# Kernel tuning notes

Hardware: AMD Instinct MI355X
Metric: run time of the kernel (lower is better)

Reference implementation:

```python
import jax, jax.numpy as jnp
import numpy as np

T, P, E, H = 256, 256, 300, 256   # seq, batch(paragraphs), embed, lstm_size
M, C = 50000, 16384               # pair occurrences / candidates per type
MT, CT = 50000, 16384             # triple occurrences / candidates


def setup_inputs() -> dict:
    key = jax.random.key(0)
    ks = jax.random.split(key, 32)
    f = lambda i, shape, s=0.05: jax.random.normal(ks[i], shape, dtype=jnp.float32) * s
    inp = {
        "x": jax.random.normal(ks[0], (T, P, E), dtype=jnp.float32),
        # BiLSTM params (pytorch gate order i,f,g,o; b = b_ih + b_hh)
        "wih_f": f(1, (4 * H, E)), "whh_f": f(2, (4 * H, H)), "b_f": f(3, (4 * H,)),
        "wih_b": f(4, (4 * H, E)), "whh_b": f(5, (4 * H, H)), "b_b": f(6, (4 * H,)),
        # per-pair-type (drug-gene, drug-variant, gene-variant) stacked params
        "pair_hW": f(7, (3, 4 * H, 2 * H)), "pair_hb": f(8, (3, 2 * H)),
        "pair_oW": f(9, (3, 2 * H)), "pair_ob": f(10, (3,)),
        "pair_backoff": f(11, (3, 2 * H)),
        "tri_hW": f(12, (6 * H, 2 * H)), "tri_hb": f(13, (2 * H,)),
        "tri_backoff": f(14, (2 * H,)),
        "all_hW": f(15, (8 * H, 2 * H)), "all_hb": f(16, (2 * H,)),
        "out_tW": f(17, (2 * H,)), "out_tb": f(18, ()),
        # flattened (t*P+p) indices of mention starts, per pair type
        "occ1": jax.random.randint(ks[19], (3, M), 0, T * P, dtype=jnp.int32),
        "occ2": jax.random.randint(ks[20], (3, M), 0, T * P, dtype=jnp.int32),
        "seg": jax.random.randint(ks[21], (3, M), 0, C, dtype=jnp.int32),
        "tri_occ1": jax.random.randint(ks[22], (MT,), 0, T * P, dtype=jnp.int32),
        "tri_occ2": jax.random.randint(ks[23], (MT,), 0, T * P, dtype=jnp.int32),
        "tri_occ3": jax.random.randint(ks[24], (MT,), 0, T * P, dtype=jnp.int32),
        "tri_seg": jax.random.randint(ks[25], (MT,), 0, CT, dtype=jnp.int32),
        # pair candidate index looked up for each triple after removing entity i
        "tri_pair_idx": jax.random.randint(ks[26], (CT, 3), 0, C, dtype=jnp.int32),
    }
    return inp


def _lstm_dir(x, wih, whh, b):
    """Unidirectional LSTM over leading time axis. x: [T, P, E] -> [T, P, H]."""
    Pb, Hh = x.shape[1], whh.shape[1]
    def step(carry, xt):
        h, c = carry
        g = xt @ wih.T + h @ whh.T + b               # [P, 4H]
        i, fgate, gg, o = jnp.split(g, 4, axis=-1)
        c = jax.nn.sigmoid(fgate) * c + jax.nn.sigmoid(i) * jnp.tanh(gg)
        h = jax.nn.sigmoid(o) * jnp.tanh(c)
        return (h, c), h
    init = (jnp.zeros((Pb, Hh), x.dtype), jnp.zeros((Pb, Hh), x.dtype))
    _, hs = jax.lax.scan(step, init, x)
    return hs


def _forward(x, wih_f, whh_f, b_f, wih_b, whh_b, b_b, pair_hW, pair_hb, pair_oW,
             pair_ob, pair_backoff, tri_hW, tri_hb, tri_backoff, all_hW, all_hb,
             out_tW, out_tb, occ1, occ2, seg, tri_occ1, tri_occ2, tri_occ3,
             tri_seg, tri_pair_idx):
    hf = _lstm_dir(x, wih_f, whh_f, b_f)
    hb = _lstm_dir(x[::-1], wih_b, whh_b, b_b)[::-1]
    embs = jnp.concatenate([hf, hb], axis=-1)        # [T, P, 2H]
    flat = embs.reshape(-1, embs.shape[-1])          # [T*P, 2H]

    pair_vecs, pair_logits = [], []
    for k in range(3):  # fixed set of entity-type pairs
        v = jnp.concatenate([flat[occ1[k]], flat[occ2[k]]], axis=-1)   # [M, 4H]
        reps = v @ pair_hW[k] + pair_hb[k]                             # [M, 2H]
        counts = jax.ops.segment_sum(jnp.ones((reps.shape[0],), reps.dtype),
                                     seg[k], num_segments=C)
        pooled = jax.ops.segment_max(reps, seg[k], num_segments=C)
        pooled = jnp.where(counts[:, None] > 0, pooled, pair_backoff[k])
        pv = jnp.tanh(pooled)                                          # [C, 2H]
        pair_vecs.append(pv)
        pair_logits.append(pv @ pair_oW[k] + pair_ob[k])               # [C]

    tv = jnp.concatenate([flat[tri_occ1], flat[tri_occ2], flat[tri_occ3]], axis=-1)
    treps = tv @ tri_hW + tri_hb                                       # [MT, 2H]
    tcounts = jax.ops.segment_sum(jnp.ones((treps.shape[0],), treps.dtype),
                                  tri_seg, num_segments=CT)
    tpooled = jax.ops.segment_max(treps, tri_seg, num_segments=CT)
    tpooled = jnp.where(tcounts[:, None] > 0, tpooled, tri_backoff)
    triple_vecs = jnp.tanh(tpooled)                                    # [CT, 2H]

    # remove drug -> (gene,variant)=type2; remove gene -> (drug,variant)=type1;
    # remove variant -> (drug,gene)=type0
    feats = jnp.concatenate([pair_vecs[2][tri_pair_idx[:, 0]],
                             pair_vecs[1][tri_pair_idx[:, 1]],
                             pair_vecs[0][tri_pair_idx[:, 2]],
                             triple_vecs], axis=1)                     # [CT, 8H]
    final = jax.nn.relu(feats @ all_hW + all_hb)
    triple_logits = final @ out_tW + out_tb                            # [CT]
    return (triple_logits, jnp.stack(pair_logits))                     # [CT], [3, C]


def reference(x, wih_f, whh_f, b_f, wih_b, whh_b, b_b, pair_hW, pair_hb, pair_oW,
              pair_ob, pair_backoff, tri_hW, tri_hb, tri_backoff, all_hW, all_hb,
              out_tW, out_tb, occ1, occ2, seg, tri_occ1, tri_occ2, tri_occ3,
              tri_seg, tri_pair_idx):
    return _forward(x, wih_f, whh_f, b_f, wih_b, whh_b, b_b, pair_hW, pair_hb,
                    pair_oW, pair_ob, pair_backoff, tri_hW, tri_hb, tri_backoff,
                    all_hW, all_hb, out_tW, out_tb, occ1, occ2, seg, tri_occ1,
                    tri_occ2, tri_occ3, tri_seg, tri_pair_idx)
```

## Files before the change

### kernel.cpp

```cpp
#include <hip/hip_runtime.h>
#include <hip/hip_bf16.h>

#define T_  256
#define P_  256
#define E_  300
#define H_  256
#define M_  50000
#define C_  16384
#define MT_ 50000
#define CT_ 16384
#define D2H 512
#define D4H 1024
#define KCH 128
#define KXW 320

#define OFF_FLAT  0ull
#define OFF_PWT   (OFF_FLAT  + (size_t)T_*P_*D2H*2)
#define OFF_TWT   (OFF_PWT   + (size_t)3*D2H*D4H*2)
#define OFF_AWT   (OFF_TWT   + (size_t)D2H*1536*2)
#define OFF_WIHT  (OFF_AWT   + (size_t)D2H*2048*2)
#define OFF_WHHB  (OFF_WIHT  + (size_t)2048*KXW*2)
#define OFF_H     (OFF_WHHB  + (size_t)2048*H_*2)
#define OFF_C     (OFF_H     + (size_t)2*2*P_*H_*4)
#define OFF_CNT   (OFF_C     + (size_t)2*P_*H_*4)
#define OFF_PPOOL (OFF_CNT   + (size_t)4*C_*4)
#define OFF_TPOOL (OFF_PPOOL + (size_t)3*C_*D2H*4)
#define WS_OLD    (OFF_TPOOL + (size_t)C_*D2H*4)
#define OFF_XW    OFF_PPOOL
#define WS_NEW    (OFF_XW    + (size_t)T_*P_*2048*2)
#define ZERO_OFF  OFF_H
#define ZERO_BYTES (WS_OLD - OFF_H)

typedef __attribute__((ext_vector_type(8))) short short8;
typedef __attribute__((ext_vector_type(4))) float floatx4;

__device__ __forceinline__ float bf2f(unsigned short u) {
    return __uint_as_float(((unsigned)u) << 16);
}
__device__ __forceinline__ unsigned short f2bf_rne(float f) {
    unsigned u = __float_as_uint(f);
    unsigned r = u + 0x7FFFu + ((u >> 16) & 1u);
    return (unsigned short)(r >> 16);
}
__device__ __forceinline__ unsigned fmap(float f) {
    unsigned u = __float_as_uint(f);
    return (u & 0x80000000u) ? ~u : (u | 0x80000000u);
}
__device__ __forceinline__ float funmap(unsigned k) {
    return __uint_as_float((k & 0x80000000u) ? (k ^ 0x80000000u) : ~k);
}
__device__ __forceinline__ float sigmoidf_(float x) { return 1.f / (1.f + __expf(-x)); }

__global__ __launch_bounds__(256) void transpose_bf16_kernel(
    const float* __restrict__ src, unsigned short* __restrict__ dst, int K, int N)
{
    __shared__ float tile[32][33];
    const int n0 = blockIdx.x << 5;
    const int k0 = blockIdx.y << 5;
    const int tx = threadIdx.x & 31;
    const int ty = threadIdx.x >> 5;
    #pragma unroll
    for (int i = 0; i < 4; ++i)
        tile[ty + (i << 3)][tx] = src[(size_t)(k0 + ty + (i << 3)) * N + n0 + tx];
    __syncthreads();
    #pragma unroll
    for (int i = 0; i < 4; ++i)
        dst[(size_t)(n0 + ty + (i << 3)) * K + k0 + tx] = f2bf_rne(tile[tx][ty + (i << 3)]);
}

__global__ __launch_bounds__(320) void wih_cast_kernel(
    const float* __restrict__ wih_f, const float* __restrict__ wih_b,
    unsigned short* __restrict__ dst)
{
    const int n = blockIdx.x;
    const int k = threadIdx.x;
    float v = 0.f;
    if (k < E_) v = (n < D4H) ? wih_f[(size_t)n * E_ + k]
                              : wih_b[(size_t)(n - D4H) * E_ + k];
    dst[(size_t)n * KXW + k] = f2bf_rne(v);
}

__global__ __launch_bounds__(256) void whh_cast_kernel(
    const float* __restrict__ whh_f, const float* __restrict__ whh_b,
    unsigned short* __restrict__ dst)
{
    const int n = blockIdx.x;
    const int k = threadIdx.x;
    const float v = (n < D4H) ? whh_f[(size_t)n * H_ + k]
                              : whh_b[(size_t)(n - D4H) * H_ + k];
    dst[(size_t)n * H_ + k] = f2bf_rne(v);
}

__global__ __launch_bounds__(256) void xw_gemm_kernel(
    const float* __restrict__ x, const unsigned short* __restrict__ wihT,
    const float* __restrict__ b_f, const float* __restrict__ b_b,
    unsigned short* __restrict__ xw)
{
    const int m0 = blockIdx.x << 5;
    const int tid = threadIdx.x;
    const int wave = tid >> 6, lane = tid & 63;
    const int n0w = (blockIdx.y << 9) + (wave << 7);
    const int lrow = lane & 15, lk = lane >> 4;

    __shared__ unsigned short At[32][KXW];

    {
        const int row = tid >> 3;
        const int c0  = (tid & 7) * 40;
        unsigned short tmp[40];
        #pragma unroll
        for (int i = 0; i < 10; ++i) {
            const int c = c0 + (i << 2);
            float4 v = {0.f, 0.f, 0.f, 0.f};
            if (c < E_) v = *(const float4*)&x[(size_t)(m0 + row) * E_ + c];
            tmp[(i << 2) + 0] = f2bf_rne(v.x);
            tmp[(i << 2) + 1] = f2bf_rne(v.y);
            tmp[(i << 2) + 2] = f2bf_rne(v.z);
            tmp[(i << 2) + 3] = f2bf_rne(v.w);
        }
        #pragma unroll
        for (int i = 0; i < 5; ++i)
            *(uint4*)&At[row][c0 + (i << 3)] = *(const uint4*)&tmp[i << 3];
    }
    __syncthreads();

    floatx4 acc[2][8] = {};
    for (int kc = 0; kc < KXW / 32; ++kc) {
        short8 af0 = *(const short8*)&At[lrow]     [(kc << 5) + (lk << 3)];
        short8 af1 = *(const short8*)&At[16 + lrow][(kc << 5) + (lk << 3)];
        const unsigned short* wb = wihT + (size_t)(n0w + lrow) * KXW + (kc << 5) + (lk << 3);
        #pragma unroll
        for (int f = 0; f < 8; ++f) {
            short8 bf = *(const short8*)(wb + (size_t)(f << 4) * KXW);
            acc[0][f] = __builtin_amdgcn_mfma_f32_16x16x32_bf16(af0, bf, acc[0][f], 0, 0, 0);
            acc[1][f] = __builtin_amdgcn_mfma_f32_16x16x32_bf16(af1, bf, acc[1][f], 0, 0, 0);
        }
    }

    #pragma unroll
    for (int f = 0; f < 8; ++f) {
        const int col = n0w + (f << 4) + lrow;
        const float bias = (col < D4H) ? b_f[col] : b_b[col - D4H];
        #pragma unroll
        for (int i = 0; i < 2; ++i)
            #pragma unroll
            for (int q = 0; q < 4; ++q) {
                const int row = m0 + (i << 4) + (lk << 2) + q;
                xw[(size_t)row * 2048 + col] = f2bf_rne(acc[i][f][q] + bias);
            }
    }
}

__global__ __launch_bounds__(256) void lstm_recur_kernel(
    const unsigned short* __restrict__ xw,
    const unsigned short* __restrict__ whhT,
    __hip_bfloat16* __restrict__ flat)
{
    const int bx  = blockIdx.x;
    const int dir = bx & 1;
    const int p0  = (bx >> 1) << 5;
    const int tid = threadIdx.x;
    const int wave = tid >> 6, lane = tid & 63;
    const int lrow = lane & 15, lk = lane >> 4;

    __shared__ unsigned short h_lds[2][32][H_];
    __shared__ unsigned short xw_lds[32][D4H];

    const unsigned short* whh = whhT + (size_t)dir * D4H * H_;

    for (int i = tid; i < 2 * 32 * H_; i += 256) ((unsigned short*)h_lds)[i] = 0;

    float cc[32];
    #pragma unroll
    for (int i = 0; i < 32; ++i) cc[i] = 0.f;
    __syncthreads();

    int cur = 0;
    for (int s = 0; s < T_; ++s) {
        const int t = dir ? (T_ - 1 - s) : s;

        {
            const unsigned short* src = xw + ((size_t)t * P_ + p0) * 2048 + dir * D4H;
            #pragma unroll
            for (int i = 0; i < 16; ++i) {
                const int idx = tid + (i << 8);
                const int row = idx >> 7;
                const int cu  = (idx & 127) << 3;
                *(uint4*)&xw_lds[row][cu] = *(const uint4*)(src + (size_t)row * 2048 + cu);
            }
        }

        floatx4 acc[2][4][4] = {};
        for (int kc = 0; kc < 8; ++kc) {
            short8 af0 = *(const short8*)&h_lds[cur][lrow]     [(kc << 5) + (lk << 3)];
            short8 af1 = *(const short8*)&h_lds[cur][16 + lrow][(kc << 5) + (lk << 3)];
            #pragma unroll
            for (int g = 0; g < 4; ++g)
                #pragma unroll
                for (int jt = 0; jt < 4; ++jt) {
                    const int nrow = (g << 8) + (wave << 6) + (jt << 4) + lrow;
                    short8 bf = *(const short8*)(whh + (size_t)nrow * H_ + (kc << 5) + (lk << 3));
                    acc[0][g][jt] = __builtin_amdgcn_mfma_f32_16x16x32_bf16(af0, bf, acc[0][g][jt], 0, 0, 0);
                    acc[1][g][jt] = __builtin_amdgcn_mfma_f32_16x16x32_bf16(af1, bf, acc[1][g][jt], 0, 0, 0);
                }
        }
        __syncthreads();

        const int nxt = cur ^ 1;
        #pragma unroll
        for (int mi = 0; mi < 2; ++mi)
            #pragma unroll
            for (int jt = 0; jt < 4; ++jt)
                #pragma unroll
                for (int q = 0; q < 4; ++q) {
                    const int j    = (wave << 6) + (jt << 4) + lrow;
                    const int ploc = (mi << 4) + (lk << 2) + q;
                    const float gi = acc[mi][0][jt][q] + bf2f(xw_lds[ploc][j]);
                    const float gf = acc[mi][1][jt][q] + bf2f(xw_lds[ploc][256 + j]);
                    const float gg = acc[mi][2][jt][q] + bf2f(xw_lds[ploc][512 + j]);
                    const float go = acc[mi][3][jt][q] + bf2f(xw_lds[ploc][768 + j]);
                    const int ci = (mi << 4) + (jt << 2) + q;
                    const float cn = sigmoidf_(gf) * cc[ci] + sigmoidf_(gi) * tanhf(gg);
                    cc[ci] = cn;
                    const float hn = sigmoidf_(go) * tanhf(cn);
                    const unsigned short hb16 = f2bf_rne(hn);
                    h_lds[nxt][ploc][j] = hb16;
                    flat[((size_t)t * P_ + p0 + ploc) * D2H + dir * H_ + j] =
                        *(const __hip_bfloat16*)&hb16;
                }
        __syncthreads();
        cur = nxt;
    }
}

__global__ __launch_bounds__(256) void lstm_step_kernel(
    const float* __restrict__ x,
    const float* __restrict__ wih_f, const float* __restrict__ whh_f, const float* __restrict__ b_f,
    const float* __restrict__ wih_b, const float* __restrict__ whh_b, const float* __restrict__ b_b,
    float* __restrict__ h_buf, float* __restrict__ c_buf,
    __hip_bfloat16* __restrict__ flat, int s)
{
    const int tid = threadIdx.x;
    const int bx  = blockIdx.x;
    const int dir = bx >> 7;
    const int rem = bx & 127;
    const int p0  = (rem >> 3) << 4;
    const int j0  = (rem & 7) << 5;
    const int t   = dir ? (T_ - 1 - s) : s;

    const float* wih = dir ? wih_b : wih_f;
    const float* whh = dir ? whh_b : whh_f;
    const float* bb  = dir ? b_b   : b_f;

    const int jj  = tid & 31;
    const int pg  = tid >> 5;
    const int pr0 = pg << 1;

    float acc[2][4] = {{0.f,0.f,0.f,0.f},{0.f,0.f,0.f,0.f}};

    __shared__ float As[16][33];
    __shared__ float Ws[32][128];

    const float* xt = x + (size_t)t * (P_ * E_);
    for (int kt = 0; kt < 10; ++kt) {
        const int kbase = kt << 5;
        {
            const int lp = tid >> 4;
            const int lkx = (tid & 15) << 1;
            #pragma unroll
            for (int i = 0; i < 2; ++i) {
                const int k = kbase + lkx + i;
                As[lp][lkx + i] = (k < E_) ? xt[(size_t)(p0 + lp) * E_ + k] : 0.f;
            }
        }
        {
            const int col  = tid >> 1;
            const int grow = ((col >> 5) * H_) + j0 + (col & 31);
            const int lk0  = (tid & 1) << 4;
            const float* wrow = wih + (size_t)grow * E_;
            #pragma unroll
            for (int i = 0; i < 16; ++i) {
                const int k = kbase + lk0 + i;
                Ws[lk0 + i][col] = (k < E_) ? wrow[k] : 0.f;
            }
        }
        __syncthreads();
        #pragma unroll
        for (int kk = 0; kk < 32; ++kk) {
            const float a0 = As[pr0][kk], a1 = As[pr0 + 1][kk];
            const float w0 = Ws[kk][jj],      w1 = Ws[kk][jj + 32];
            const float w2 = Ws[kk][jj + 64], w3 = Ws[kk][jj + 96];
            acc[0][0] = fmaf(a0, w0, acc[0][0]); acc[0][1] = fmaf(a0, w1, acc[0][1]);
            acc[0][2] = fmaf(a0, w2, acc[0][2]); acc[0][3] = fmaf(a0, w3, acc[0][3]);
            acc[1][0] = fmaf(a1, w0, acc[1][0]); acc[1][1] = fmaf(a1, w1, acc[1][1]);
            acc[1][2] = fmaf(a1, w2, acc[1][2]); acc[1][3] = fmaf(a1, w3, acc[1][3]);
        }
        __syncthreads();
    }

    const float* hprev = h_buf + (size_t)((s & 1) * 2 + dir) * (P_ * H_);
    for (int kt = 0; kt < 8; ++kt) {
        const int kbase = kt << 5;
        {
            const int lp = tid >> 4;
            const int lkx = (tid & 15) << 1;
            #pragma unroll
            for (int i = 0; i < 2; ++i)
                As[lp][lkx + i] = hprev[(size_t)(p0 + lp) * H_ + kbase + lkx + i];
        }
        {
            const int col  = tid >> 1;
            const int grow = ((col >> 5) * H_) + j0 + (col & 31);
            const int lk0  = (tid & 1) << 4;
            const float* wrow = whh + (size_t)grow * H_;
            #pragma unroll
            for (int i = 0; i < 16; ++i)
                Ws[lk0 + i][col] = wrow[kbase + lk0 + i];
        }
        __syncthreads();
        #pragma unroll
        for (int kk = 0; kk < 32; ++kk) {
            const float a0 = As[pr0][kk], a1 = As[pr0 + 1][kk];
            const float w0 = Ws[kk][jj],      w1 = Ws[kk][jj + 32];
            const float w2 = Ws[kk][jj + 64], w3 = Ws[kk][jj + 96];
            acc[0][0] = fmaf(a0, w0, acc[0][0]); acc[0][1] = fmaf(a0, w1, acc[0][1]);
            acc[0][2] = fmaf(a0, w2, acc[0][2]); acc[0][3] = fmaf(a0, w3, acc[0][3]);
            acc[1][0] = fmaf(a1, w0, acc[1][0]); acc[1][1] = fmaf(a1, w1, acc[1][1]);
            acc[1][2] = fmaf(a1, w2, acc[1][2]); acc[1][3] = fmaf(a1, w3, acc[1][3]);
        }
        __syncthreads();
    }

    const int j = j0 + jj;
    const float bi = bb[j], bfv = bb[H_ + j], bgv = bb[2 * H_ + j], bo = bb[3 * H_ + j];
    float* hnew = h_buf + (size_t)(((s & 1) ^ 1) * 2 + dir) * (P_ * H_);
    float* cst  = c_buf + (size_t)dir * (P_ * H_);
    #pragma unroll
    for (int i = 0; i < 2; ++i) {
        const int p = p0 + pr0 + i;
        const float gi = acc[i][0] + bi;
        const float gf = acc[i][1] + bfv;
        const float gg = acc[i][2] + bgv;
        const float go = acc[i][3] + bo;
        const size_t off = (size_t)p * H_ + j;
        const float cold = cst[off];
        const float cn = sigmoidf_(gf) * cold + sigmoidf_(gi) * tanhf(gg);
        const float hn = sigmoidf_(go) * tanhf(cn);
        cst[off]  = cn;
        hnew[off] = hn;
        flat[((size_t)t * P_ + p) * D2H + dir * H_ + j] = __float2bfloat16(hn);
    }
}

__global__ __launch_bounds__(256) void pair_mfma_kernel(
    const unsigned short* __restrict__ flat,
    const unsigned short* __restrict__ Wt,
    const float* __restrict__ hb,
    const int* __restrict__ occ1, const int* __restrict__ occ2,
    const int* __restrict__ seg,
    unsigned* __restrict__ pooled)
{
    const int type = blockIdx.z;
    const int m0 = blockIdx.x << 5;
    const int tid = threadIdx.x;
    const int wave = tid >> 6, lane = tid & 63;
    const int n0w = wave << 7;
    const int lrow = lane & 15, lk = lane >> 4;

    const unsigned short* W = Wt + (size_t)type * D2H * D4H;

    __shared__ unsigned short At[32][KCH + 8];
    floatx4 acc[2][8] = {};

    const int srow = tid >> 3;
    const int scol = (tid & 7) << 4;
    const int r = m0 + srow;
    const bool rv = (r < M_);
    const int i1 = rv ? occ1[type * M_ + r] : 0;
    const int i2 = rv ? occ2[type * M_ + r] : 0;

    for (int kc = 0; kc < D4H / KCH; ++kc) {
        {
            const int kg  = kc * KCH + scol;
            const int src = (kg < 512) ? i1 : i2;
            const int col = kg & 511;
            const unsigned short* p = flat + (size_t)src * D2H + col;
            *(uint4*)&At[srow][scol]     = *(const uint4*)p;
            *(uint4*)&At[srow][scol + 8] = *(const uint4*)(p + 8);
        }
        __syncthreads();
        #pragma unroll
        for (int ks = 0; ks < KCH / 32; ++ks) {
            short8 af0 = *(const short8*)&At[lrow]     [(ks << 5) + (lk << 3)];
            short8 af1 = *(const short8*)&At[16 + lrow][(ks << 5) + (lk << 3)];
            const int kgb = kc * KCH + (ks << 5) + (lk << 3);
            const unsigned short* wb = W + (size_t)(n0w + lrow) * D4H + kgb;
            #pragma unroll
            for (int f = 0; f < 8; ++f) {
                short8 bf = *(const short8*)(wb + (size_t)(f << 4) * D4H);
                acc[0][f] = __builtin_amdgcn_mfma_f32_16x16x32_bf16(af0, bf, acc[0][f], 0, 0, 0);
                acc[1][f] = __builtin_amdgcn_mfma_f32_16x16x32_bf16(af1, bf, acc[1][f], 0, 0, 0);
            }
        }
        __syncthreads();
    }

    int segs[2][4];
    #pragma unroll
    for (int i = 0; i < 2; ++i)
        #pragma unroll
        for (int q = 0; q < 4; ++q) {
            const int row = m0 + (i << 4) + (lk << 2) + q;
            segs[i][q] = (row < M_) ? seg[type * M_ + row] : -1;
        }
    #pragma unroll
    for (int f = 0; f < 8; ++f) {
        const int col = n0w + (f << 4) + lrow;
        const float bias = hb[type * D2H + col];
        #pragma unroll
        for (int i = 0; i < 2; ++i)
            #pragma unroll
            for (int q = 0; q < 4; ++q) {
                if (segs[i][q] < 0) continue;
                atomicMax(pooled + ((size_t)type * C_ + segs[i][q]) * D2H + col,
                          fmap(acc[i][f][q] + bias));
            }
    }
}

__global__ __launch_bounds__(256) void tri_mfma_kernel(
    const unsigned short* __restrict__ flat,
    const unsigned short* __restrict__ Wt,
    const float* __restrict__ hb,
    const int* __restrict__ o1, const int* __restrict__ o2, const int* __restrict__ o3,
    const int* __restrict__ seg,
    unsigned* __restrict__ pooled)
{
    const int m0 = blockIdx.x << 5;
    const int tid = threadIdx.x;
    const int wave = tid >> 6, lane = tid & 63;
    const int n0w = wave << 7;
    const int lrow = lane & 15, lk = lane >> 4;
    const int K = 1536;

    __shared__ unsigned short At[32][KCH + 8];
    floatx4 acc[2][8] = {};

    const int srow = tid >> 3;
    const int scol = (tid & 7) << 4;
    const int r = m0 + srow;
    const bool rv = (r < MT_);
    const int i1 = rv ? o1[r] : 0;
    const int i2 = rv ? o2[r] : 0;
    const int i3 = rv ? o3[r] : 0;

    for (int kc = 0; kc < 12; ++kc) {
        {
            const int kg  = kc * KCH + scol;
            const int src = (kg < 512) ? i1 : (kg < 1024 ? i2 : i3);
            const int col = kg & 511;
            const unsigned short* p = flat + (size_t)src * D2H + col;
            *(uint4*)&At[srow][scol]     = *(const uint4*)p;
            *(uint4*)&At[srow][scol + 8] = *(const uint4*)(p + 8);
        }
        __syncthreads();
        #pragma unroll
        for (int ks = 0; ks < KCH / 32; ++ks) {
            short8 af0 = *(const short8*)&At[lrow]     [(ks << 5) + (lk << 3)];
            short8 af1 = *(const short8*)&At[16 + lrow][(ks << 5) + (lk << 3)];
            const int kgb = kc * KCH + (ks << 5) + (lk << 3);
            const unsigned short* wb = Wt + (size_t)(n0w + lrow) * K + kgb;
            #pragma unroll
            for (int f = 0; f < 8; ++f) {
                short8 bf = *(const short8*)(wb + (size_t)(f << 4) * K);
                acc[0][f] = __builtin_amdgcn_mfma_f32_16x16x32_bf16(af0, bf, acc[0][f], 0, 0, 0);
                acc[1][f] = __builtin_amdgcn_mfma_f32_16x16x32_bf16(af1, bf, acc[1][f], 0, 0, 0);
            }
        }
        __syncthreads();
    }

    int segs[2][4];
    #pragma unroll
    for (int i = 0; i < 2; ++i)
        #pragma unroll
        for (int q = 0; q < 4; ++q) {
            const int row = m0 + (i << 4) + (lk << 2) + q;
            segs[i][q] = (row < MT_) ? seg[row] : -1;
        }
    #pragma unroll
    for (int f = 0; f < 8; ++f) {
        const int col = n0w + (f << 4) + lrow;
        const float bias = hb[col];
        #pragma unroll
        for (int i = 0; i < 2; ++i)
            #pragma unroll
            for (int q = 0; q < 4; ++q) {
                if (segs[i][q] < 0) continue;
                atomicMax(pooled + (size_t)segs[i][q] * D2H + col,
                          fmap(acc[i][f][q] + bias));
            }
    }
}

__global__ void counts_kernel(const int* __restrict__ seg, const int* __restrict__ tri_seg,
                              int* __restrict__ counts)
{
    const int i = blockIdx.x * 256 + threadIdx.x;
    if (i < 3 * M_) {
        atomicAdd(&counts[(i / M_) * C_ + seg[i]], 1);
    } else {
        const int m = i - 3 * M_;
        if (m < MT_) atomicAdd(&counts[3 * C_ + tri_seg[m]], 1);
    }
}

__global__ __launch_bounds__(256) void pair_finalize_kernel(
    unsigned* __restrict__ pooled, const int* __restrict__ counts,
    const float* __restrict__ backoff, const float* __restrict__ oW,
    const float* __restrict__ ob, float* __restrict__ out)
{
    const int lane = threadIdx.x & 63;
    const int idx  = (blockIdx.x << 2) + (threadIdx.x >> 6);
    const int type = idx / C_;
    unsigned* row = pooled + (size_t)idx * D2H;
    const int cnt = counts[idx];
    float sum = 0.f;
    #pragma unroll
    for (int q = 0; q < 8; ++q) {
        const int col = (q << 6) + lane;
        const float v = (cnt > 0) ? funmap(row[col]) : backoff[type * D2H + col];
        const float pvv = tanhf(v);
        ((float*)row)[col] = pvv;
        sum += pvv * oW[type * D2H + col];
    }
    #pragma unroll
    for (int off = 32; off > 0; off >>= 1) sum += __shfl_down(sum, off);
    if (lane == 0) out[CT_ + idx] = sum + ob[type];
}

__global__ void tri_finalize_kernel(unsigned* __restrict__ tpool,
                                    const int* __restrict__ counts,
                                    const float* __restrict__ tri_backoff)
{
    const int gid = blockIdx.x * 256 + threadIdx.x;
    const int c = gid >> 9, col = gid & 511;
    const float v = (counts[3 * C_ + c] > 0) ? funmap(tpool[gid]) : tri_backoff[col];
    ((float*)tpool)[gid] = tanhf(v);
}

__global__ __launch_bounds__(256) void final_mfma_kernel(
    const float* __restrict__ pv,
    const float* __restrict__ trv,
    const unsigned short* __restrict__ Wt,
    const float* __restrict__ all_hb,
    const float* __restrict__ out_tW, const float* __restrict__ out_tb,
    const int* __restrict__ tpi,
    float* __restrict__ out)
{
    const int m0 = blockIdx.x << 5;
    const int tid = threadIdx.x;
    const int wave = tid >> 6, lane = tid & 63;
    const int n0w = wave << 7;
    const int lrow = lane & 15, lk = lane >> 4;
    const int K = 2048;

    __shared__ unsigned short At[32][KCH + 8];
    __shared__ float wpart[4][32];
    floatx4 acc[2][8] = {};

    const int srow = tid >> 3;
    const int scol = (tid & 7) << 4;
    const int r = m0 + srow;
    const float* srcs[4];
    srcs[0] = pv  + ((size_t)2 * C_ + tpi[r * 3 + 0]) * D2H;
    srcs[1] = pv  + ((size_t)1 * C_ + tpi[r * 3 + 1]) * D2H;
    srcs[2] = pv  + ((size_t)0 * C_ + tpi[r * 3 + 2]) * D2H;
    srcs[3] = trv + (size_t)r * D2H;

    for (int kc = 0; kc < 16; ++kc) {
        {
            const int kg  = kc * KCH + scol;
            const float* p = srcs[kg >> 9] + (kg & 511);
            unsigned short tmp[16];
            #pragma unroll
            for (int v4 = 0; v4 < 4; ++v4) {
                const float4 fv = *(const float4*)(p + (v4 << 2));
                tmp[v4 * 4 + 0] = f2bf_rne(fv.x);
                tmp[v4 * 4 + 1] = f2bf_rne(fv.y);
                tmp[v4 * 4 + 2] = f2bf_rne(fv.z);
                tmp[v4 * 4 + 3] = f2bf_rne(fv.w);
            }
            *(uint4*)&At[srow][scol]     = *(const uint4*)&tmp[0];
            *(uint4*)&At[srow][scol + 8] = *(const uint4*)&tmp[8];
        }
        __syncthreads();
        #pragma unroll
        for (int ks = 0; ks < KCH / 32; ++ks) {
            short8 af0 = *(const short8*)&At[lrow]     [(ks << 5) + (lk << 3)];
            short8 af1 = *(const short8*)&At[16 + lrow][(ks << 5) + (lk << 3)];
            const int kgb = kc * KCH + (ks << 5) + (lk << 3);
            const unsigned short* wb = Wt + (size_t)(n0w + lrow) * K + kgb;
            #pragma unroll
            for (int f = 0; f < 8; ++f) {
                short8 bf = *(const short8*)(wb + (size_t)(f << 4) * K);
                acc[0][f] = __builtin_amdgcn_mfma_f32_16x16x32_bf16(af0, bf, acc[0][f], 0, 0, 0);
                acc[1][f] = __builtin_amdgcn_mfma_f32_16x16x32_bf16(af1, bf, acc[1][f], 0, 0, 0);
            }
        }
        __syncthreads();
    }

    float psum[2][4] = {{0,0,0,0},{0,0,0,0}};
    #pragma unroll
    for (int f = 0; f < 8; ++f) {
        const int col = n0w + (f << 4) + lrow;
        const float bias = all_hb[col];
        const float w = out_tW[col];
        #pragma unroll
        for (int i = 0; i < 2; ++i)
            #pragma unroll
            for (int q = 0; q < 4; ++q)
                psum[i][q] = fmaf(fmaxf(acc[i][f][q] + bias, 0.f), w, psum[i][q]);
    }
    #pragma unroll
    for (int i = 0; i < 2; ++i)
        #pragma unroll
        for (int q = 0; q < 4; ++q) {
            float s = psum[i][q];
            s += __shfl_xor(s, 1); s += __shfl_xor(s, 2);
            s += __shfl_xor(s, 4); s += __shfl_xor(s, 8);
            if (lrow == 0) wpart[wave][(i << 4) + (lk << 2) + q] = s;
        }
    __syncthreads();
    if (tid < 32)
        out[m0 + tid] = wpart[0][tid] + wpart[1][tid] + wpart[2][tid] + wpart[3][tid]
                        + out_tb[0];
}

extern "C" void kernel_launch(void* const* d_in, const int* in_sizes, int n_in,
                              void* d_out, int out_size, void* d_ws, size_t ws_size,
                              hipStream_t stream)
{
    const float* x        = (const float*)d_in[0];
    const float* wih_f    = (const float*)d_in[1];
    const float* whh_f    = (const float*)d_in[2];
    const float* b_f      = (const float*)d_in[3];
    const float* wih_b    = (const float*)d_in[4];
    const float* whh_b    = (const float*)d_in[5];
    const float* b_b      = (const float*)d_in[6];
    const float* pair_hW  = (const float*)d_in[7];
    const float* pair_hb  = (const float*)d_in[8];
    const float* pair_oW  = (const float*)d_in[9];
    const float* pair_ob  = (const float*)d_in[10];
    const float* pair_bo  = (const float*)d_in[11];
    const float* tri_hW   = (const float*)d_in[12];
    const float* tri_hb   = (const float*)d_in[13];
    const float* tri_bo   = (const float*)d_in[14];
    const float* all_hW   = (const float*)d_in[15];
    const float* all_hb   = (const float*)d_in[16];
    const float* out_tW   = (const float*)d_in[17];
    const float* out_tb   = (const float*)d_in[18];
    const int*   occ1     = (const int*)d_in[19];
    const int*   occ2     = (const int*)d_in[20];
    const int*   seg      = (const int*)d_in[21];
    const int*   tri_occ1 = (const int*)d_in[22];
    const int*   tri_occ2 = (const int*)d_in[23];
    const int*   tri_occ3 = (const int*)d_in[24];
    const int*   tri_seg  = (const int*)d_in[25];
    const int*   tpi      = (const int*)d_in[26];

    if (ws_size < WS_OLD) return;

    char* ws = (char*)d_ws;
    __hip_bfloat16* flat = (__hip_bfloat16*)(ws + OFF_FLAT);
    unsigned short* pwt  = (unsigned short*)(ws + OFF_PWT);
    unsigned short* twt  = (unsigned short*)(ws + OFF_TWT);
    unsigned short* awt  = (unsigned short*)(ws + OFF_AWT);
    unsigned short* wihT = (unsigned short*)(ws + OFF_WIHT);
    unsigned short* whhB = (unsigned short*)(ws + OFF_WHHB);
    float*    h_buf      = (float*)(ws + OFF_H);
    float*    c_buf      = (float*)(ws + OFF_C);
    int*      counts     = (int*)(ws + OFF_CNT);
    unsigned* ppool      = (unsigned*)(ws + OFF_PPOOL);
    unsigned* tpool      = (unsigned*)(ws + OFF_TPOOL);
    unsigned short* xw   = (unsigned short*)(ws + OFF_XW);
    float*    out        = (float*)d_out;

    const bool fast = (ws_size >= WS_NEW);

    for (int t = 0; t < 3; ++t)
        transpose_bf16_kernel<<<dim3(D2H / 32, D4H / 32), 256, 0, stream>>>(
            pair_hW + (size_t)t * D4H * D2H, pwt + (size_t)t * D2H * D4H, D4H, D2H);
    transpose_bf16_kernel<<<dim3(D2H / 32, 1536 / 32), 256, 0, stream>>>(tri_hW, twt, 1536, D2H);
    transpose_bf16_kernel<<<dim3(D2H / 32, 2048 / 32), 256, 0, stream>>>(all_hW, awt, 2048, D2H);

    if (fast) {
        wih_cast_kernel<<<2048, 320, 0, stream>>>(wih_f, wih_b, wihT);
        whh_cast_kernel<<<2048, 256, 0, stream>>>(whh_f, whh_b, whhB);
        xw_gemm_kernel<<<dim3(T_ * P_ / 32, 4), 256, 0, stream>>>(x, wihT, b_f, b_b, xw);
        lstm_recur_kernel<<<16, 256, 0, stream>>>(xw, whhB, flat);
        hipMemsetAsync(ws + ZERO_OFF, 0, ZERO_BYTES, stream);
    } else {
        hipMemsetAsync(ws + ZERO_OFF, 0, ZERO_BYTES, stream);
        for (int s = 0; s < T_; ++s)
            lstm_step_kernel<<<256, 256, 0, stream>>>(x, wih_f, whh_f, b_f,
                                                      wih_b, whh_b, b_b,
                                                      h_buf, c_buf, flat, s);
    }

    pair_mfma_kernel<<<dim3((M_ + 31) / 32, 1, 3), 256, 0, stream>>>(
        (const unsigned short*)flat, pwt, pair_hb, occ1, occ2, seg, ppool);
    tri_mfma_kernel<<<dim3((MT_ + 31) / 32), 256, 0, stream>>>(
        (const unsigned short*)flat, twt, tri_hb, tri_occ1, tri_occ2, tri_occ3, tri_seg, tpool);
    counts_kernel<<<(3 * M_ + MT_ + 255) / 256, 256, 0, stream>>>(seg, tri_seg, counts);

    pair_finalize_kernel<<<(3 * C_) / 4, 256, 0, stream>>>(
        ppool, counts, pair_bo, pair_oW, pair_ob, out);
    tri_finalize_kernel<<<(CT_ * D2H) / 256, 256, 0, stream>>>(tpool, counts, tri_bo);

    final_mfma_kernel<<<CT_ / 32, 256, 0, stream>>>(
        (const float*)ppool, (const float*)tpool, awt, all_hb, out_tW, out_tb, tpi, out);
}
```

Baseline: 9.057 ms.

## Chunk input projection and LSTM recurrence over batch halves to fit workspace

The full input-projection buffer is split into two batch halves of 128 paragraphs. Each half is computed by the bf16 MFMA GEMM and then consumed by the fused recurrence kernel, so the scratch reuses the pooling region. This removes the workspace-size gate and the fallback of 256 per-timestep fp32 launches, so the MFMA path always runs. The cost is that the two recurrences run one after the other with only 8 blocks each, which serialises the latency-bound loop.

```diff
diff --git a/kernel.cpp b/kernel.cpp
--- a/kernel.cpp
+++ b/kernel.cpp
@@ -13,6 +13,7 @@
 #define D4H 1024
 #define KCH 128
 #define KXW 320
+#define PCHK 128
 
 #define OFF_FLAT  0ull
 #define OFF_PWT   (OFF_FLAT  + (size_t)T_*P_*D2H*2)
@@ -25,11 +26,10 @@
 #define OFF_CNT   (OFF_C     + (size_t)2*P_*H_*4)
 #define OFF_PPOOL (OFF_CNT   + (size_t)4*C_*4)
 #define OFF_TPOOL (OFF_PPOOL + (size_t)3*C_*D2H*4)
-#define WS_OLD    (OFF_TPOOL + (size_t)C_*D2H*4)
-#define OFF_XW    OFF_PPOOL
-#define WS_NEW    (OFF_XW    + (size_t)T_*P_*2048*2)
+#define WS_NEED   (OFF_TPOOL + (size_t)C_*D2H*4)
+#define OFF_XWB   OFF_PPOOL
 #define ZERO_OFF  OFF_H
-#define ZERO_BYTES (WS_OLD - OFF_H)
+#define ZERO_BYTES (WS_NEED - OFF_H)
 
 typedef __attribute__((ext_vector_type(8))) short short8;
 typedef __attribute__((ext_vector_type(4))) float floatx4;
@@ -94,7 +94,7 @@
 __global__ __launch_bounds__(256) void xw_gemm_kernel(
     const float* __restrict__ x, const unsigned short* __restrict__ wihT,
     const float* __restrict__ b_f, const float* __restrict__ b_b,
-    unsigned short* __restrict__ xw)
+    unsigned short* __restrict__ xwb, int chunk)
 {
     const int m0 = blockIdx.x << 5;
     const int tid = threadIdx.x;
@@ -106,13 +106,17 @@
 
     {
         const int row = tid >> 3;
+        const int gm  = m0 + row;
+        const int t   = gm >> 7;
+        const int pl  = gm & (PCHK - 1);
+        const float* xrow = x + ((size_t)t * P_ + (chunk << 7) + pl) * E_;
         const int c0  = (tid & 7) * 40;
         unsigned short tmp[40];
         #pragma unroll
         for (int i = 0; i < 10; ++i) {
             const int c = c0 + (i << 2);
             float4 v = {0.f, 0.f, 0.f, 0.f};
-            if (c < E_) v = *(const float4*)&x[(size_t)(m0 + row) * E_ + c];
+            if (c < E_) v = *(const float4*)&xrow[c];
             tmp[(i << 2) + 0] = f2bf_rne(v.x);
             tmp[(i << 2) + 1] = f2bf_rne(v.y);
             tmp[(i << 2) + 2] = f2bf_rne(v.z);
@@ -146,19 +150,20 @@
             #pragma unroll
             for (int q = 0; q < 4; ++q) {
                 const int row = m0 + (i << 4) + (lk << 2) + q;
-                xw[(size_t)row * 2048 + col] = f2bf_rne(acc[i][f][q] + bias);
+                xwb[(size_t)row * 2048 + col] = f2bf_rne(acc[i][f][q] + bias);
             }
     }
 }
 
 __global__ __launch_bounds__(256) void lstm_recur_kernel(
-    const unsigned short* __restrict__ xw,
+    const unsigned short* __restrict__ xwb,
     const unsigned short* __restrict__ whhT,
-    __hip_bfloat16* __restrict__ flat)
+    __hip_bfloat16* __restrict__ flat, int chunk)
 {
     const int bx  = blockIdx.x;
     const int dir = bx & 1;
-    const int p0  = (bx >> 1) << 5;
+    const int pl0 = (bx >> 1) << 5;
+    const int p0  = (chunk << 7) + pl0;
     const int tid = threadIdx.x;
     const int wave = tid >> 6, lane = tid & 63;
     const int lrow = lane & 15, lk = lane >> 4;
@@ -180,7 +185,7 @@
         const int t = dir ? (T_ - 1 - s) : s;
 
         {
-            const unsigned short* src = xw + ((size_t)t * P_ + p0) * 2048 + dir * D4H;
+            const unsigned short* src = xwb + ((size_t)t * PCHK + pl0) * 2048 + dir * D4H;
             #pragma unroll
             for (int i = 0; i < 16; ++i) {
                 const int idx = tid + (i << 8);
@@ -230,125 +235,6 @@
                 }
         __syncthreads();
         cur = nxt;
-    }
-}
-
-__global__ __launch_bounds__(256) void lstm_step_kernel(
-    const float* __restrict__ x,
-    const float* __restrict__ wih_f, const float* __restrict__ whh_f, const float* __restrict__ b_f,
-    const float* __restrict__ wih_b, const float* __restrict__ whh_b, const float* __restrict__ b_b,
-    float* __restrict__ h_buf, float* __restrict__ c_buf,
-    __hip_bfloat16* __restrict__ flat, int s)
-{
-    const int tid = threadIdx.x;
-    const int bx  = blockIdx.x;
-    const int dir = bx >> 7;
-    const int rem = bx & 127;
-    const int p0  = (rem >> 3) << 4;
-    const int j0  = (rem & 7) << 5;
-    const int t   = dir ? (T_ - 1 - s) : s;
-
-    const float* wih = dir ? wih_b : wih_f;
-    const float* whh = dir ? whh_b : whh_f;
-    const float* bb  = dir ? b_b   : b_f;
-
-    const int jj  = tid & 31;
-    const int pg  = tid >> 5;
-    const int pr0 = pg << 1;
-
-    float acc[2][4] = {{0.f,0.f,0.f,0.f},{0.f,0.f,0.f,0.f}};
-
-    __shared__ float As[16][33];
-    __shared__ float Ws[32][128];
-
-    const float* xt = x + (size_t)t * (P_ * E_);
-    for (int kt = 0; kt < 10; ++kt) {
-        const int kbase = kt << 5;
-        {
-            const int lp = tid >> 4;
-            const int lkx = (tid & 15) << 1;
-            #pragma unroll
-            for (int i = 0; i < 2; ++i) {
-                const int k = kbase + lkx + i;
-                As[lp][lkx + i] = (k < E_) ? xt[(size_t)(p0 + lp) * E_ + k] : 0.f;
-            }
-        }
-        {
-            const int col  = tid >> 1;
-            const int grow = ((col >> 5) * H_) + j0 + (col & 31);
-            const int lk0  = (tid & 1) << 4;
-            const float* wrow = wih + (size_t)grow * E_;
-            #pragma unroll
-            for (int i = 0; i < 16; ++i) {
-                const int k = kbase + lk0 + i;
-                Ws[lk0 + i][col] = (k < E_) ? wrow[k] : 0.f;
-            }
-        }
-        __syncthreads();
-        #pragma unroll
-        for (int kk = 0; kk < 32; ++kk) {
-            const float a0 = As[pr0][kk], a1 = As[pr0 + 1][kk];
-            const float w0 = Ws[kk][jj],      w1 = Ws[kk][jj + 32];
-            const float w2 = Ws[kk][jj + 64], w3 = Ws[kk][jj + 96];
-            acc[0][0] = fmaf(a0, w0, acc[0][0]); acc[0][1] = fmaf(a0, w1, acc[0][1]);
-            acc[0][2] = fmaf(a0, w2, acc[0][2]); acc[0][3] = fmaf(a0, w3, acc[0][3]);
-            acc[1][0] = fmaf(a1, w0, acc[1][0]); acc[1][1] = fmaf(a1, w1, acc[1][1]);
-            acc[1][2] = fmaf(a1, w2, acc[1][2]); acc[1][3] = fmaf(a1, w3, acc[1][3]);
-        }
-        __syncthreads();
-    }
-
-    const float* hprev = h_buf + (size_t)((s & 1) * 2 + dir) * (P_ * H_);
-    for (int kt = 0; kt < 8; ++kt) {
-        const int kbase = kt << 5;
-        {
-            const int lp = tid >> 4;
-            const int lkx = (tid & 15) << 1;
-            #pragma unroll
-            for (int i = 0; i < 2; ++i)
-                As[lp][lkx + i] = hprev[(size_t)(p0 + lp) * H_ + kbase + lkx + i];
-        }
-        {
-            const int col  = tid >> 1;
-            const int grow = ((col >> 5) * H_) + j0 + (col & 31);
-            const int lk0  = (tid & 1) << 4;
-            const float* wrow = whh + (size_t)grow * H_;
-            #pragma unroll
-            for (int i = 0; i < 16; ++i)
-                Ws[lk0 + i][col] = wrow[kbase + lk0 + i];
-        }
-        __syncthreads();
-        #pragma unroll
-        for (int kk = 0; kk < 32; ++kk) {
-            const float a0 = As[pr0][kk], a1 = As[pr0 + 1][kk];
-            const float w0 = Ws[kk][jj],      w1 = Ws[kk][jj + 32];
-            const float w2 = Ws[kk][jj + 64], w3 = Ws[kk][jj + 96];
-            acc[0][0] = fmaf(a0, w0, acc[0][0]); acc[0][1] = fmaf(a0, w1, acc[0][1]);
-            acc[0][2] = fmaf(a0, w2, acc[0][2]); acc[0][3] = fmaf(a0, w3, acc[0][3]);
-            acc[1][0] = fmaf(a1, w0, acc[1][0]); acc[1][1] = fmaf(a1, w1, acc[1][1]);
-            acc[1][2] = fmaf(a1, w2, acc[1][2]); acc[1][3] = fmaf(a1, w3, acc[1][3]);
-        }
-        __syncthreads();
-    }
-
-    const int j = j0 + jj;
-    const float bi = bb[j], bfv = bb[H_ + j], bgv = bb[2 * H_ + j], bo = bb[3 * H_ + j];
-    float* hnew = h_buf + (size_t)(((s & 1) ^ 1) * 2 + dir) * (P_ * H_);
-    float* cst  = c_buf + (size_t)dir * (P_ * H_);
-    #pragma unroll
-    for (int i = 0; i < 2; ++i) {
-        const int p = p0 + pr0 + i;
-        const float gi = acc[i][0] + bi;
-        const float gf = acc[i][1] + bfv;
-        const float gg = acc[i][2] + bgv;
-        const float go = acc[i][3] + bo;
-        const size_t off = (size_t)p * H_ + j;
-        const float cold = cst[off];
-        const float cn = sigmoidf_(gf) * cold + sigmoidf_(gi) * tanhf(gg);
-        const float hn = sigmoidf_(go) * tanhf(cn);
-        cst[off]  = cn;
-        hnew[off] = hn;
-        flat[((size_t)t * P_ + p) * D2H + dir * H_ + j] = __float2bfloat16(hn);
     }
 }
 
@@ -670,7 +556,7 @@
     const int*   tri_seg  = (const int*)d_in[25];
     const int*   tpi      = (const int*)d_in[26];
 
-    if (ws_size < WS_OLD) return;
+    if (ws_size < WS_NEED) return;
 
     char* ws = (char*)d_ws;
     __hip_bfloat16* flat = (__hip_bfloat16*)(ws + OFF_FLAT);
@@ -679,35 +565,27 @@
     unsigned short* awt  = (unsigned short*)(ws + OFF_AWT);
     unsigned short* wihT = (unsigned short*)(ws + OFF_WIHT);
     unsigned short* whhB = (unsigned short*)(ws + OFF_WHHB);
-    float*    h_buf      = (float*)(ws + OFF_H);
-    float*    c_buf      = (float*)(ws + OFF_C);
     int*      counts     = (int*)(ws + OFF_CNT);
     unsigned* ppool      = (unsigned*)(ws + OFF_PPOOL);
     unsigned* tpool      = (unsigned*)(ws + OFF_TPOOL);
-    unsigned short* xw   = (unsigned short*)(ws + OFF_XW);
+    unsigned short* xwb  = (unsigned short*)(ws + OFF_XWB);
     float*    out        = (float*)d_out;
-
-    const bool fast = (ws_size >= WS_NEW);
 
     for (int t = 0; t < 3; ++t)
         transpose_bf16_kernel<<<dim3(D2H / 32, D4H / 32), 256, 0, stream>>>(
             pair_hW + (size_t)t * D4H * D2H, pwt + (size_t)t * D2H * D4H, D4H, D2H);
     transpose_bf16_kernel<<<dim3(D2H / 32, 1536 / 32), 256, 0, stream>>>(tri_hW, twt, 1536, D2H);
     transpose_bf16_kernel<<<dim3(D2H / 32, 2048 / 32), 256, 0, stream>>>(all_hW, awt, 2048, D2H);
-
-    if (fast) {
-        wih_cast_kernel<<<2048, 320, 0, stream>>>(wih_f, wih_b, wihT);
-        whh_cast_kernel<<<2048, 256, 0, stream>>>(whh_f, whh_b, whhB);
-        xw_gemm_kernel<<<dim3(T_ * P_ / 32, 4), 256, 0, stream>>>(x, wihT, b_f, b_b, xw);
-        lstm_recur_kernel<<<16, 256, 0, stream>>>(xw, whhB, flat);
-        hipMemsetAsync(ws + ZERO_OFF, 0, ZERO_BYTES, stream);
-    } else {
-        hipMemsetAsync(ws + ZERO_OFF, 0, ZERO_BYTES, stream);
-        for (int s = 0; s < T_; ++s)
-            lstm_step_kernel<<<256, 256, 0, stream>>>(x, wih_f, whh_f, b_f,
-                                                      wih_b, whh_b, b_b,
-                                                      h_buf, c_buf, flat, s);
-    }
+    wih_cast_kernel<<<2048, 320, 0, stream>>>(wih_f, wih_b, wihT);
+    whh_cast_kernel<<<2048, 256, 0, stream>>>(whh_f, whh_b, whhB);
+
+    for (int chunk = 0; chunk < 2; ++chunk) {
+        xw_gemm_kernel<<<dim3(T_ * PCHK / 32, 4), 256, 0, stream>>>(
+            x, wihT, b_f, b_b, xwb, chunk);
+        lstm_recur_kernel<<<8, 256, 0, stream>>>(xwb, whhB, flat, chunk);
+    }
+
+    hipMemsetAsync(ws + ZERO_OFF, 0, ZERO_BYTES, stream);
 
     pair_mfma_kernel<<<dim3((M_ + 31) / 32, 1, 3), 256, 0, stream>>>(
         (const unsigned short*)flat, pwt, pair_hb, occ1, occ2, seg, ppool);
```

Result: slower. 14.79 ms (+63.2%).
